# Performance work log

Measured on AMD Instinct MI355X. Metric: run time of the kernel, lower is better.

## Reference

```python
import jax, jax.numpy as jnp
import numpy as np

B, C, H, W = 2, 512, 30, 40
K = 64
PATCH, STRIDE = 4, 1
EPS = 1e-12  # torch F.normalize eps


def _l2norm(v, axis):
    n = jnp.sqrt(jnp.sum(v * v, axis=axis, keepdims=True))
    return v / jnp.maximum(n, EPS)


def setup_inputs() -> dict:
    key = jax.random.key(0)
    k1, k2, k3 = jax.random.split(key, 3)
    x = jax.random.normal(k1, (B, C, H, W), dtype=jnp.float32)
    conv_w = jax.random.normal(k2, (K, C), dtype=jnp.float32) * 0.05  # 1x1 conv weight, no bias (vlad_v2=False)
    centroids = jax.random.normal(k3, (K, C), dtype=jnp.float32)
    return {"x": x, "conv_w": conv_w, "centroids": centroids}


def reference(x, conv_w, centroids):
    b, c, h, w = x.shape
    k = centroids.shape[0]
    # input L2 normalization along channels
    xn = _l2norm(x, axis=1)
    # soft assignment: 1x1 conv + softmax over clusters
    soft = jax.nn.softmax(jnp.einsum('kc,bchw->bkhw', conv_w, xn), axis=1)
    # weighted residuals [B,K,C,H,W] (fused; original loops over K)
    resid = (xn[:, None, :, :, :] - centroids[None, :, :, None, None]) * soft[:, :, None, :, :]
    # global VLAD: sum over spatial
    vlad_global = jnp.sum(resid, axis=(-2, -1))  # [B,K,C]
    vlad_global = _l2norm(vlad_global, axis=2).reshape(b, -1)
    vlad_global = _l2norm(vlad_global, axis=1)
    # integral image over [B, K*C, H, W]
    r = resid.reshape(b, k * c, h, w)
    integ = jnp.cumsum(jnp.cumsum(r, axis=-1), axis=-2)
    integ = jnp.pad(integ, ((0, 0), (0, 0), (1, 0), (1, 0)))  # [B,KC,H+1,W+1]
    # box-sum via integral-image differences (equiv. to the dilated 2x2 grouped conv)
    p, s = PATCH, STRIDE
    hp = (h - p) // s + 1
    wp = (w - p) // s + 1
    ye, xe = (hp - 1) * s + 1, (wp - 1) * s + 1
    tl = integ[:, :, 0:ye:s, 0:xe:s]
    tr = integ[:, :, 0:ye:s, p:p + xe:s]
    bl = integ[:, :, p:p + ye:s, 0:xe:s]
    br = integ[:, :, p:p + ye:s, p:p + xe:s]
    box = (br - tr - bl + tl) / (p * p)  # [B,KC,hp,wp]
    v = box.reshape(b, k, c, hp * wp)
    v = _l2norm(v, axis=2)  # intra-cluster norm
    v = v.reshape(b, k * c, hp * wp)
    vlad_local = _l2norm(v, axis=1)  # [B, K*C, hp*wp]
    return (vlad_local, vlad_global)
```

## Files before the change

### kernel.cpp

```cpp
#include <hip/hip_runtime.h>
#include <math.h>

#define BB 2
#define CC 512
#define HH 30
#define WW 40
#define KK 64
#define NPIX (HH*WW)
#define HP 27
#define WP 37
#define NP (HP*WP)
#define LEPS 1e-12f

#define PADW 168
#define SROW 680
#define NCG 8

__global__ __launch_bounds__(512) void k_norm_soft(
    const float* __restrict__ x, const float* __restrict__ convw,
    float* __restrict__ xn, float* __restrict__ soft)
{
  const int h = blockIdx.x, b = blockIdx.y;
  const int t = threadIdx.x;
  __shared__ float xc[64][41];
  __shared__ float cw[64][65];
  __shared__ float Lb[KK][WW + 1];
  __shared__ float psum[12][WW];
  __shared__ float invn[WW];
  __shared__ float mx[WW], Zs[WW];

  const size_t xbase = (size_t)b * CC * NPIX + (size_t)h * WW;

  if (t < 480) {
    const int w = t % 40, part = t / 40;
    float s = 0.f;
    for (int c = part; c < CC; c += 12) {
      const float v = x[xbase + (size_t)c * NPIX + w];
      s = fmaf(v, v, s);
    }
    psum[part][w] = s;
  }
  __syncthreads();
  if (t < 40) {
    float s = 0.f;
    #pragma unroll
    for (int p = 0; p < 12; ++p) s += psum[p][t];
    invn[t] = 1.f / fmaxf(sqrtf(s), LEPS);
  }
  __syncthreads();

  const int k = t & 63, wp = t >> 6;
  float acc[5] = {0.f, 0.f, 0.f, 0.f, 0.f};
  for (int cb = 0; cb < CC; cb += 64) {
    #pragma unroll
    for (int n = 0; n < 5; ++n) {
      const int idx = t + 512 * n;
      const int c = idx / 40, w = idx % 40;
      const float v = x[xbase + (size_t)(cb + c) * NPIX + w] * invn[w];
      xc[c][w] = v;
      xn[xbase + (size_t)(cb + c) * NPIX + w] = v;
    }
    #pragma unroll
    for (int n = 0; n < 8; ++n) {
      const int idx = t + 512 * n;
      const int kk2 = idx >> 6, c2 = idx & 63;
      cw[kk2][c2] = convw[(size_t)kk2 * CC + cb + c2];
    }
    __syncthreads();
    #pragma unroll 1
    for (int c = 0; c < 64; ++c) {
      const float cv = cw[k][c];
      #pragma unroll
      for (int n = 0; n < 5; ++n)
        acc[n] = fmaf(cv, xc[c][wp + 8 * n], acc[n]);
    }
    __syncthreads();
  }
  #pragma unroll
  for (int n = 0; n < 5; ++n) Lb[k][wp + 8 * n] = acc[n];
  __syncthreads();
  if (t < 40) {
    float m = -1e30f;
    for (int kk2 = 0; kk2 < KK; ++kk2) m = fmaxf(m, Lb[kk2][t]);
    float Z = 0.f;
    for (int kk2 = 0; kk2 < KK; ++kk2) Z += expf(Lb[kk2][t] - m);
    mx[t] = m; Zs[t] = Z;
  }
  __syncthreads();
  const size_t sbase = (size_t)b * KK * NPIX + (size_t)h * WW;
  #pragma unroll
  for (int n = 0; n < 5; ++n) {
    const int idx = t + 512 * n;
    const int kk2 = idx / 40, w = idx % 40;
    soft[sbase + (size_t)kk2 * NPIX + w] = expf(Lb[kk2][w] - mx[w]) / Zs[w];
  }
}

__global__ __launch_bounds__(256) void k_global(
    const float* __restrict__ xn, const float* __restrict__ soft,
    const float* __restrict__ cent, float* __restrict__ ghat)
{
  const int k = blockIdx.x, b = blockIdx.y, t = threadIdx.x;
  __shared__ float sb[NPIX];
  __shared__ float red[256];
  const float* srow = soft + ((size_t)b * KK + k) * NPIX;
  for (int i2 = t; i2 < NPIX; i2 += 256) sb[i2] = srow[i2];
  __syncthreads();
  float p = 0.f;
  for (int i2 = t; i2 < NPIX; i2 += 256) p += sb[i2];
  red[t] = p;
  __syncthreads();
  for (int s = 128; s > 0; s >>= 1) { if (t < s) red[t] += red[t + s]; __syncthreads(); }
  const float Sg = red[0];
  __syncthreads();

  const int c0 = t, c1 = t + 256;
  const float* x0 = xn + ((size_t)b * CC + c0) * NPIX;
  const float* x1 = xn + ((size_t)b * CC + c1) * NPIX;
  float a0 = 0.f, a1 = 0.f;
  for (int p4 = 0; p4 < NPIX; p4 += 4) {
    const float4 s4 = *(const float4*)&sb[p4];
    const float4 v0 = *(const float4*)(x0 + p4);
    const float4 v1 = *(const float4*)(x1 + p4);
    a0 = fmaf(s4.x, v0.x, a0); a0 = fmaf(s4.y, v0.y, a0);
    a0 = fmaf(s4.z, v0.z, a0); a0 = fmaf(s4.w, v0.w, a0);
    a1 = fmaf(s4.x, v1.x, a1); a1 = fmaf(s4.y, v1.y, a1);
    a1 = fmaf(s4.z, v1.z, a1); a1 = fmaf(s4.w, v1.w, a1);
  }
  const float g0 = a0 - cent[(size_t)k * CC + c0] * Sg;
  const float g1 = a1 - cent[(size_t)k * CC + c1] * Sg;
  red[t] = g0 * g0 + g1 * g1;
  __syncthreads();
  for (int s = 128; s > 0; s >>= 1) { if (t < s) red[t] += red[t + s]; __syncthreads(); }
  const float inv = 1.f / fmaxf(sqrtf(red[0]), LEPS);
  float* gr = ghat + ((size_t)b * KK + k) * CC;
  gr[c0] = g0 * inv; gr[c1] = g1 * inv;
}

__global__ __launch_bounds__(256) void k_g2a(
    const float* __restrict__ ghat, float* __restrict__ inv2g)
{
  const int b = blockIdx.x, t = threadIdx.x;
  __shared__ float red[256];
  const float* gb = ghat + (size_t)b * KK * CC;
  float p = 0.f;
  for (int i2 = t; i2 < KK * CC; i2 += 256) { const float v = gb[i2]; p = fmaf(v, v, p); }
  red[t] = p;
  __syncthreads();
  for (int s = 128; s > 0; s >>= 1) { if (t < s) red[t] += red[t + s]; __syncthreads(); }
  if (t == 0) inv2g[b] = 1.f / fmaxf(sqrtf(red[0]), LEPS);
}

__global__ __launch_bounds__(256) void k_g2b(
    const float* __restrict__ ghat, const float* __restrict__ inv2g,
    float* __restrict__ outg)
{
  const int b = blockIdx.y;
  const int u = blockIdx.x * 256 + threadIdx.x;
  if (u < KK * CC)
    outg[(size_t)b * KK * CC + u] = ghat[(size_t)b * KK * CC + u] * inv2g[b];
}

__global__ __launch_bounds__(320, 2) void k_rawssq(
    const float* __restrict__ xn, const float* __restrict__ soft,
    const float* __restrict__ cent, float* __restrict__ sp,
    float* __restrict__ out)
{
  const int cg = blockIdx.x;
  const int k0 = blockIdx.y * 4;
  const int bz = blockIdx.z;
  const int b = bz >> 1, iz = bz & 1;
  const int i0 = iz * 14;
  const int n_i = iz ? 13 : 14;
  const int c0 = cg * 64;
  const int t = threadIdx.x;
  const int c8 = t / 40, j = t % 40;

  __shared__ float xn_l[64][PADW];
  __shared__ float soft_l[4][SROW];
  __shared__ float cent_l[4][64];
  __shared__ float red[8 * 4 * 40];

  {
    const int len = (NPIX - i0 * 40) < SROW ? (NPIX - i0 * 40) : SROW;
    const int nf4 = len >> 2;
    for (int u = t; u < 4 * nf4; u += 320) {
      const int kk = u / nf4, q = u - kk * nf4;
      *(float4*)&soft_l[kk][q * 4] =
        *(const float4*)&soft[((size_t)(b * KK + k0 + kk)) * NPIX + i0 * 40 + q * 4];
    }
  }
  if (t < 256) cent_l[t >> 6][t & 63] = cent[(size_t)(k0 + (t >> 6)) * CC + c0 + (t & 63)];

  const int sc = t / 10, sq = t % 10;
  #pragma unroll
  for (int rr = 0; rr < 4; ++rr) {
    const int row = i0 + rr;
    const int slot = (row & 3) * 40 + sq * 4;
    *(float4*)&xn_l[sc][slot] =
      *(const float4*)&xn[((size_t)(b * CC + c0 + sc)) * NPIX + (size_t)row * 40 + sq * 4];
    *(float4*)&xn_l[sc + 32][slot] =
      *(const float4*)&xn[((size_t)(b * CC + c0 + sc + 32)) * NPIX + (size_t)row * 40 + sq * 4];
  }
  __syncthreads();

  for (int ii = 0; ii < n_i; ++ii) {
    const int i = i0 + ii;

    const int nrow = (i + 4 < HH) ? (i + 4) : (HH - 1);
    const float4 st0 = *(const float4*)&xn[((size_t)(b * CC + c0 + sc)) * NPIX
                                           + (size_t)nrow * 40 + sq * 4];
    const float4 st1 = *(const float4*)&xn[((size_t)(b * CC + c0 + sc + 32)) * NPIX
                                           + (size_t)nrow * 40 + sq * 4];

    float sloc[4] = {0.f, 0.f, 0.f, 0.f};
    if (j < WP) {
      float acc[8][4];
      float Ssum[4] = {0.f, 0.f, 0.f, 0.f};
      #pragma unroll
      for (int cc = 0; cc < 8; ++cc)
        #pragma unroll
        for (int kk = 0; kk < 4; ++kk) acc[cc][kk] = 0.f;
      #pragma unroll
      for (int r = 0; r < 4; ++r) {
        const int xo = ((i + r) & 3) * 40 + j;
        const int so = (ii + r) * 40 + j;
        float sv[4][4];
        #pragma unroll
        for (int kk = 0; kk < 4; ++kk) {
          #pragma unroll
          for (int dx = 0; dx < 4; ++dx) sv[kk][dx] = soft_l[kk][so + dx];
          Ssum[kk] += (sv[kk][0] + sv[kk][1]) + (sv[kk][2] + sv[kk][3]);
        }
        #pragma unroll
        for (int cc = 0; cc < 8; ++cc) {
          const float x0 = xn_l[c8 * 8 + cc][xo + 0];
          const float x1 = xn_l[c8 * 8 + cc][xo + 1];
          const float x2 = xn_l[c8 * 8 + cc][xo + 2];
          const float x3 = xn_l[c8 * 8 + cc][xo + 3];
          #pragma unroll
          for (int kk = 0; kk < 4; ++kk) {
            float a = acc[cc][kk];
            a = fmaf(x0, sv[kk][0], a);
            a = fmaf(x1, sv[kk][1], a);
            a = fmaf(x2, sv[kk][2], a);
            a = fmaf(x3, sv[kk][3], a);
            acc[cc][kk] = a;
          }
        }
      }
      #pragma unroll
      for (int kk = 0; kk < 4; ++kk) {
        const float Sv = Ssum[kk];
        #pragma unroll
        for (int cc = 0; cc < 8; ++cc) {
          const float raw = fmaf(-cent_l[kk][c8 * 8 + cc], Sv, acc[cc][kk]);
          sloc[kk] = fmaf(raw, raw, sloc[kk]);
          out[((size_t)((b * KK + k0 + kk) * CC + c0 + c8 * 8 + cc)) * NP
              + (size_t)i * WP + j] = raw;
        }
      }
    }
    #pragma unroll
    for (int kk = 0; kk < 4; ++kk) red[(c8 * 4 + kk) * 40 + j] = sloc[kk];
    __syncthreads();

    {
      const int slot = ((i + 4) & 3) * 40 + sq * 4;
      *(float4*)&xn_l[sc][slot] = st0;
      *(float4*)&xn_l[sc + 32][slot] = st1;
    }
    if (t < 160) {
      const int kk = t / 40, jj = t % 40;
      if (jj < WP) {
        float s = 0.f;
        #pragma unroll
        for (int g = 0; g < 8; ++g) s += red[(g * 4 + kk) * 40 + jj];
        sp[(((size_t)(b * KK + k0 + kk)) * NCG + cg) * NP + (size_t)i * WP + jj] = s;
      }
    }
    __syncthreads();
  }
}

__global__ __launch_bounds__(256) void k_nf(
    const float* __restrict__ sp, float* __restrict__ fs)
{
  const int b = blockIdx.y, t = threadIdx.x;
  const int k = t >> 2, dp = t & 3;
  const int p = blockIdx.x * 4 + dp;
  __shared__ float red[64][4];
  __shared__ float inv2s[4];
  const bool ok = p < NP;
  float sr = 0.f;
  if (ok) {
    #pragma unroll
    for (int g = 0; g < NCG; ++g)
      sr += sp[(((size_t)(b * KK + k)) * NCG + g) * NP + p];
  }
  const float iv = 1.f / fmaxf(sqrtf(sr) * 0.0625f, LEPS);
  red[k][dp] = sr * (1.f / 256.f) * iv * iv;
  __syncthreads();
  if (t < 4) {
    float s = 0.f;
    #pragma unroll
    for (int kk = 0; kk < 64; ++kk) s += red[kk][t];
    inv2s[t] = 1.f / fmaxf(sqrtf(s), LEPS);
  }
  __syncthreads();
  if (ok)
    fs[((size_t)(b * KK + k)) * NP + p] = 0.0625f * iv * inv2s[dp];
}

__global__ __launch_bounds__(256) void k_scale(
    float* __restrict__ outr, const float* __restrict__ fs)
{
  const size_t NV = (size_t)BB * KK * CC * NP / 4;
  const int CPN = CC * NP;
  for (size_t v = (size_t)blockIdx.x * 256 + threadIdx.x; v < NV;
       v += (size_t)gridDim.x * 256) {
    const size_t base = v * 4;
    const int bk = (int)(base / CPN);
    const int rem = (int)(base - (size_t)bk * CPN);
    int p0 = rem % NP;
    const float* fb = fs + (size_t)bk * NP;
    const int p1 = (p0 + 1 == NP) ? 0 : p0 + 1;
    const int p2 = (p1 + 1 == NP) ? 0 : p1 + 1;
    const int p3 = (p2 + 1 == NP) ? 0 : p2 + 1;
    float4 o = *(float4*)&outr[base];
    o.x *= fb[p0]; o.y *= fb[p1]; o.z *= fb[p2]; o.w *= fb[p3];
    *(float4*)&outr[base] = o;
  }
}

extern "C" void kernel_launch(void* const* d_in, const int* in_sizes, int n_in,
                              void* d_out, int out_size, void* d_ws, size_t ws_size,
                              hipStream_t stream)
{
  const float* x     = (const float*)d_in[0];
  const float* convw = (const float*)d_in[1];
  const float* cent  = (const float*)d_in[2];
  float* out = (float*)d_out;
  float* ws  = (float*)d_ws;

  float* xn    = ws;
  float* soft  = xn    + (size_t)BB * CC * NPIX;
  float* fs    = soft  + (size_t)BB * KK * NPIX;
  float* ghat  = fs    + (size_t)BB * KK * NP;
  float* sp    = ghat  + (size_t)BB * KK * CC;
  float* inv2g = sp    + (size_t)BB * KK * NCG * NP;

  float* outg = out + (size_t)BB * KK * CC * NP;

  k_norm_soft<<<dim3(HH, BB), 512, 0, stream>>>(x, convw, xn, soft);
  k_rawssq<<<dim3(NCG, KK / 4, BB * 2), 320, 0, stream>>>(xn, soft, cent, sp, out);
  k_global<<<dim3(KK, BB), 256, 0, stream>>>(xn, soft, cent, ghat);
  k_g2a<<<dim3(BB), 256, 0, stream>>>(ghat, inv2g);
  k_g2b<<<dim3((KK * CC + 255) / 256, BB), 256, 0, stream>>>(ghat, inv2g, outg);
  k_nf<<<dim3((NP + 3) / 4, BB), 256, 0, stream>>>(sp, fs);
  k_scale<<<dim3(2048), 256, 0, stream>>>(out, fs);
}
```

Measured before the change: 415.8 us.

## Fuse output scaling into recomputed second local pass, drop k_scale

Splits the local box-sum kernel into two template phases: phase 0 computes only the per-pixel sum-of-squares partials, and phase 1 recomputes the box sums and writes them pre-multiplied by the normalization factor. This removes the separate read-modify-write scaling pass over the large local output, trading it for recomputing the FMAs. It also remaps threads so that the channel index varies fastest, using wave shuffles instead of a shared-memory reduction, and splits rows into three chunks with higher occupancy. The new mapping may reduce store coalescing, since consecutive lanes now write to different channel rows.

```diff
diff --git a/kernel.cpp b/kernel.cpp
--- a/kernel.cpp
+++ b/kernel.cpp
@@ -12,8 +12,8 @@
 #define NP (HP*WP)
 #define LEPS 1e-12f
 
-#define PADW 168
-#define SROW 680
+#define PADW 164
+#define SROW 484
 #define NCG 8
 
 __global__ __launch_bounds__(512) void k_norm_soft(
@@ -161,34 +161,29 @@
     outg[(size_t)b * KK * CC + u] = ghat[(size_t)b * KK * CC + u] * inv2g[b];
 }
 
-__global__ __launch_bounds__(320, 2) void k_rawssq(
+template<int PHASE>
+__global__ __launch_bounds__(320, 3) void k_local7(
     const float* __restrict__ xn, const float* __restrict__ soft,
     const float* __restrict__ cent, float* __restrict__ sp,
-    float* __restrict__ out)
+    const float* __restrict__ fs, float* __restrict__ out)
 {
   const int cg = blockIdx.x;
   const int k0 = blockIdx.y * 4;
   const int bz = blockIdx.z;
-  const int b = bz >> 1, iz = bz & 1;
-  const int i0 = iz * 14;
-  const int n_i = iz ? 13 : 14;
+  const int b = bz / 3, iz = bz % 3;
+  const int i0 = iz * 9;
   const int c0 = cg * 64;
   const int t = threadIdx.x;
-  const int c8 = t / 40, j = t % 40;
+  const int c8 = t & 7, j = t >> 3;
 
   __shared__ float xn_l[64][PADW];
   __shared__ float soft_l[4][SROW];
   __shared__ float cent_l[4][64];
-  __shared__ float red[8 * 4 * 40];
-
-  {
-    const int len = (NPIX - i0 * 40) < SROW ? (NPIX - i0 * 40) : SROW;
-    const int nf4 = len >> 2;
-    for (int u = t; u < 4 * nf4; u += 320) {
-      const int kk = u / nf4, q = u - kk * nf4;
-      *(float4*)&soft_l[kk][q * 4] =
-        *(const float4*)&soft[((size_t)(b * KK + k0 + kk)) * NPIX + i0 * 40 + q * 4];
-    }
+
+  for (int u = t; u < 480; u += 320) {
+    const int kk = u / 120, q = u - (u / 120) * 120;
+    *(float4*)&soft_l[kk][q * 4] =
+      *(const float4*)&soft[((size_t)(b * KK + k0 + kk)) * NPIX + i0 * 40 + q * 4];
   }
   if (t < 256) cent_l[t >> 6][t & 63] = cent[(size_t)(k0 + (t >> 6)) * CC + c0 + (t & 63)];
 
@@ -204,7 +199,7 @@
   }
   __syncthreads();
 
-  for (int ii = 0; ii < n_i; ++ii) {
+  for (int ii = 0; ii < 9; ++ii) {
     const int i = i0 + ii;
 
     const int nrow = (i + 4 < HH) ? (i + 4) : (HH - 1);
@@ -212,72 +207,81 @@
                                            + (size_t)nrow * 40 + sq * 4];
     const float4 st1 = *(const float4*)&xn[((size_t)(b * CC + c0 + sc + 32)) * NPIX
                                            + (size_t)nrow * 40 + sq * 4];
-
-    float sloc[4] = {0.f, 0.f, 0.f, 0.f};
-    if (j < WP) {
-      float acc[8][4];
-      float Ssum[4] = {0.f, 0.f, 0.f, 0.f};
-      #pragma unroll
-      for (int cc = 0; cc < 8; ++cc)
+    float fsv[4];
+    if (PHASE == 1) {
+      #pragma unroll
+      for (int kk = 0; kk < 4; ++kk)
+        fsv[kk] = (j < WP)
+          ? fs[((size_t)(b * KK + k0 + kk)) * NP + (size_t)i * WP + j] : 0.f;
+    }
+
+    float acc[8][4];
+    float Ssum[4] = {0.f, 0.f, 0.f, 0.f};
+    #pragma unroll
+    for (int cc = 0; cc < 8; ++cc)
+      #pragma unroll
+      for (int kk = 0; kk < 4; ++kk) acc[cc][kk] = 0.f;
+    #pragma unroll
+    for (int r = 0; r < 4; ++r) {
+      const int xo = ((i + r) & 3) * 40 + j;
+      const int so = (ii + r) * 40 + j;
+      float sv[4][4];
+      #pragma unroll
+      for (int kk = 0; kk < 4; ++kk) {
         #pragma unroll
-        for (int kk = 0; kk < 4; ++kk) acc[cc][kk] = 0.f;
-      #pragma unroll
-      for (int r = 0; r < 4; ++r) {
-        const int xo = ((i + r) & 3) * 40 + j;
-        const int so = (ii + r) * 40 + j;
-        float sv[4][4];
+        for (int dx = 0; dx < 4; ++dx) sv[kk][dx] = soft_l[kk][so + dx];
+        Ssum[kk] += (sv[kk][0] + sv[kk][1]) + (sv[kk][2] + sv[kk][3]);
+      }
+      #pragma unroll
+      for (int cc = 0; cc < 8; ++cc) {
+        const float x0 = xn_l[cc * 8 + c8][xo + 0];
+        const float x1 = xn_l[cc * 8 + c8][xo + 1];
+        const float x2 = xn_l[cc * 8 + c8][xo + 2];
+        const float x3 = xn_l[cc * 8 + c8][xo + 3];
         #pragma unroll
         for (int kk = 0; kk < 4; ++kk) {
-          #pragma unroll
-          for (int dx = 0; dx < 4; ++dx) sv[kk][dx] = soft_l[kk][so + dx];
-          Ssum[kk] += (sv[kk][0] + sv[kk][1]) + (sv[kk][2] + sv[kk][3]);
+          float a = acc[cc][kk];
+          a = fmaf(x0, sv[kk][0], a);
+          a = fmaf(x1, sv[kk][1], a);
+          a = fmaf(x2, sv[kk][2], a);
+          a = fmaf(x3, sv[kk][3], a);
+          acc[cc][kk] = a;
         }
+      }
+    }
+
+    if (PHASE == 0) {
+      #pragma unroll
+      for (int kk = 0; kk < 4; ++kk) {
+        float s = 0.f;
         #pragma unroll
         for (int cc = 0; cc < 8; ++cc) {
-          const float x0 = xn_l[c8 * 8 + cc][xo + 0];
-          const float x1 = xn_l[c8 * 8 + cc][xo + 1];
-          const float x2 = xn_l[c8 * 8 + cc][xo + 2];
-          const float x3 = xn_l[c8 * 8 + cc][xo + 3];
-          #pragma unroll
-          for (int kk = 0; kk < 4; ++kk) {
-            float a = acc[cc][kk];
-            a = fmaf(x0, sv[kk][0], a);
-            a = fmaf(x1, sv[kk][1], a);
-            a = fmaf(x2, sv[kk][2], a);
-            a = fmaf(x3, sv[kk][3], a);
-            acc[cc][kk] = a;
-          }
+          const float raw = fmaf(-cent_l[kk][cc * 8 + c8], Ssum[kk], acc[cc][kk]);
+          s = fmaf(raw, raw, s);
+        }
+        s += __shfl_xor(s, 1, 64);
+        s += __shfl_xor(s, 2, 64);
+        s += __shfl_xor(s, 4, 64);
+        if (c8 == 0 && j < WP)
+          sp[(((size_t)(b * KK + k0 + kk)) * NCG + cg) * NP + (size_t)i * WP + j] = s;
+      }
+    } else if (j < WP) {
+      #pragma unroll
+      for (int kk = 0; kk < 4; ++kk) {
+        #pragma unroll
+        for (int cc = 0; cc < 8; ++cc) {
+          const float raw = fmaf(-cent_l[kk][cc * 8 + c8], Ssum[kk], acc[cc][kk]);
+          out[((size_t)((b * KK + k0 + kk) * CC + c0 + cc * 8 + c8)) * NP
+              + (size_t)i * WP + j] = raw * fsv[kk];
         }
       }
-      #pragma unroll
-      for (int kk = 0; kk < 4; ++kk) {
-        const float Sv = Ssum[kk];
-        #pragma unroll
-        for (int cc = 0; cc < 8; ++cc) {
-          const float raw = fmaf(-cent_l[kk][c8 * 8 + cc], Sv, acc[cc][kk]);
-          sloc[kk] = fmaf(raw, raw, sloc[kk]);
-          out[((size_t)((b * KK + k0 + kk) * CC + c0 + c8 * 8 + cc)) * NP
-              + (size_t)i * WP + j] = raw;
-        }
-      }
-    }
-    #pragma unroll
-    for (int kk = 0; kk < 4; ++kk) red[(c8 * 4 + kk) * 40 + j] = sloc[kk];
+    }
     __syncthreads();
 
     {
       const int slot = ((i + 4) & 3) * 40 + sq * 4;
       *(float4*)&xn_l[sc][slot] = st0;
       *(float4*)&xn_l[sc + 32][slot] = st1;
-    }
-    if (t < 160) {
-      const int kk = t / 40, jj = t % 40;
-      if (jj < WP) {
-        float s = 0.f;
-        #pragma unroll
-        for (int g = 0; g < 8; ++g) s += red[(g * 4 + kk) * 40 + jj];
-        sp[(((size_t)(b * KK + k0 + kk)) * NCG + cg) * NP + (size_t)i * WP + jj] = s;
-      }
     }
     __syncthreads();
   }
@@ -312,27 +316,6 @@
     fs[((size_t)(b * KK + k)) * NP + p] = 0.0625f * iv * inv2s[dp];
 }
 
-__global__ __launch_bounds__(256) void k_scale(
-    float* __restrict__ outr, const float* __restrict__ fs)
-{
-  const size_t NV = (size_t)BB * KK * CC * NP / 4;
-  const int CPN = CC * NP;
-  for (size_t v = (size_t)blockIdx.x * 256 + threadIdx.x; v < NV;
-       v += (size_t)gridDim.x * 256) {
-    const size_t base = v * 4;
-    const int bk = (int)(base / CPN);
-    const int rem = (int)(base - (size_t)bk * CPN);
-    int p0 = rem % NP;
-    const float* fb = fs + (size_t)bk * NP;
-    const int p1 = (p0 + 1 == NP) ? 0 : p0 + 1;
-    const int p2 = (p1 + 1 == NP) ? 0 : p1 + 1;
-    const int p3 = (p2 + 1 == NP) ? 0 : p2 + 1;
-    float4 o = *(float4*)&outr[base];
-    o.x *= fb[p0]; o.y *= fb[p1]; o.z *= fb[p2]; o.w *= fb[p3];
-    *(float4*)&outr[base] = o;
-  }
-}
-
 extern "C" void kernel_launch(void* const* d_in, const int* in_sizes, int n_in,
                               void* d_out, int out_size, void* d_ws, size_t ws_size,
                               hipStream_t stream)
@@ -353,10 +336,10 @@
   float* outg = out + (size_t)BB * KK * CC * NP;
 
   k_norm_soft<<<dim3(HH, BB), 512, 0, stream>>>(x, convw, xn, soft);
-  k_rawssq<<<dim3(NCG, KK / 4, BB * 2), 320, 0, stream>>>(xn, soft, cent, sp, out);
+  k_local7<0><<<dim3(NCG, KK / 4, BB * 3), 320, 0, stream>>>(xn, soft, cent, sp, fs, out);
   k_global<<<dim3(KK, BB), 256, 0, stream>>>(xn, soft, cent, ghat);
   k_g2a<<<dim3(BB), 256, 0, stream>>>(ghat, inv2g);
   k_g2b<<<dim3((KK * CC + 255) / 256, BB), 256, 0, stream>>>(ghat, inv2g, outg);
   k_nf<<<dim3((NP + 3) / 4, BB), 256, 0, stream>>>(sp, fs);
-  k_scale<<<dim3(2048), 256, 0, stream>>>(out, fs);
-}
+  k_local7<1><<<dim3(NCG, KK / 4, BB * 3), 320, 0, stream>>>(xn, soft, cent, sp, fs, out);
+}
```

Result: slower. 556.9 us (+33.9%).
